# Kernel optimization log

Measured on AMD Instinct MI355X. Metric: run time of the kernel, lower is better.

## Reference

```python
import jax, jax.numpy as jnp
import numpy as np

N_NODES = 100000
N_EDGES = 1600000
N_GRAPHS = 256
F_IN = 38
HID = 64


def graph_conv(x, edge_index, w_rel, b_rel, w_root):
    # PyG GraphConv (aggr='add'): out = lin_rel(sum_{j in N(i)} x_j) + lin_root(x_i)
    src, dst = edge_index[0], edge_index[1]
    agg = jax.ops.segment_sum(x[src], dst, num_segments=N_NODES)  # [N, F]
    return agg @ w_rel + b_rel + x @ w_root


def setup_inputs() -> dict:
    key = jax.random.key(0)
    ks = jax.random.split(key, 10)
    x = jax.random.normal(ks[0], (N_NODES, F_IN), dtype=jnp.float32)
    edge_index = jax.random.randint(ks[1], (2, N_EDGES), 0, N_NODES, dtype=jnp.int64)
    batch = jnp.sort(jax.random.randint(ks[2], (N_NODES,), 0, N_GRAPHS, dtype=jnp.int64))
    s1 = 1.0 / np.sqrt(F_IN)
    s2 = 1.0 / np.sqrt(HID)
    w1_rel = jax.random.uniform(ks[3], (F_IN, HID), jnp.float32, -s1, s1)
    b1_rel = jax.random.uniform(ks[4], (HID,), jnp.float32, -s1, s1)
    w1_root = jax.random.uniform(ks[5], (F_IN, HID), jnp.float32, -s1, s1)
    w2_rel = jax.random.uniform(ks[6], (HID, HID), jnp.float32, -s2, s2)
    b2_rel = jax.random.uniform(ks[7], (HID,), jnp.float32, -s2, s2)
    w2_root = jax.random.uniform(ks[8], (HID, HID), jnp.float32, -s2, s2)
    return {"x": x, "edge_index": edge_index, "batch": batch,
            "w1_rel": w1_rel, "b1_rel": b1_rel, "w1_root": w1_root,
            "w2_rel": w2_rel, "b2_rel": b2_rel, "w2_root": w2_root}


def reference(x, edge_index, batch, w1_rel, b1_rel, w1_root, w2_rel, b2_rel, w2_root):
    h = graph_conv(x, edge_index, w1_rel, b1_rel, w1_root)
    h = jax.nn.relu(h)
    h = graph_conv(h, edge_index, w2_rel, b2_rel, w2_root)
    # global_mean_pool: segment mean over batch ids
    sums = jax.ops.segment_sum(h, batch, num_segments=N_GRAPHS)  # [G, HID]
    counts = jax.ops.segment_sum(jnp.ones((N_NODES,), h.dtype), batch, num_segments=N_GRAPHS)
    pooled = sums / jnp.maximum(counts, 1.0)[:, None]
    # dropout(p=0.5, training=False) is identity in eval mode
    return jax.nn.relu(pooled)
```

## Files before the change

### kernel.cpp

```cpp
#include <hip/hip_runtime.h>

#define N_NODES 100000
#define N_EDGES 1600000
#define N_GRAPHS 256
#define F_IN 38
#define F_PAD 40
#define HID 64
#define CAPD 48

#define NB   391
#define EPB  4096
#define EDGE_BLOCKS 391
#define PACK_BLOCKS 1024
#define PACK_CHUNKS ((N_NODES + 1) * F_PAD / 8)
#define BCAP 4608
#define NBL  (2 * NB)

typedef unsigned short ushort;
typedef unsigned int uint;
typedef _Float16 h2 __attribute__((ext_vector_type(2)));

__device__ __forceinline__ h2 u2h(uint u) {
    union { uint u; h2 h; } v; v.u = u; return v.h;
}
__device__ __forceinline__ uint h2u(h2 h) {
    union { uint u; h2 h; } v; v.h = h; return v.u;
}
__device__ __forceinline__ ushort f2h_bits(float f) {
    union { _Float16 h; ushort s; } v; v.h = (_Float16)f; return v.s;
}
__device__ __forceinline__ int clampi(int v) {
    return (int)min((uint)v, (uint)N_NODES);
}

__global__ __launch_bounds__(256, 4) void pre_kernel(
        const float* __restrict__ x,
        const int* __restrict__ src,
        const int* __restrict__ dst,
        int* __restrict__ gcur,
        uint* __restrict__ ebuf,
        ushort* __restrict__ xb,
        ushort* __restrict__ hb) {
    __shared__ int    hist[NB];
    __shared__ int    offs[NB];
    __shared__ int    cur[NB];
    __shared__ int    gbase[NB];
    __shared__ int    scan[512];
    __shared__ uint   sbuf[EPB];
    __shared__ ushort sb[EPB];

    const int blk = blockIdx.x;
    if (blk >= EDGE_BLOCKS) {
        int gid = (blk - EDGE_BLOCKS) * 256 + threadIdx.x;
        if (gid < HID) hb[(N_NODES << 6) + gid] = 0;
        const int stride = PACK_BLOCKS * 256;
        for (int c = gid; c < PACK_CHUNKS; c += stride) {
            int n = c / 5;
            int f0 = (c - n * 5) * 8;
            ushort u[8];
            #pragma unroll
            for (int j = 0; j < 8; ++j) {
                int f = f0 + j;
                float v = (n < N_NODES && f < F_IN) ? x[n * F_IN + f] : 0.0f;
                u[j] = f2h_bits(v);
            }
            uint4 pk;
            pk.x = (uint)u[0] | ((uint)u[1] << 16);
            pk.y = (uint)u[2] | ((uint)u[3] << 16);
            pk.z = (uint)u[4] | ((uint)u[5] << 16);
            pk.w = (uint)u[6] | ((uint)u[7] << 16);
            *(uint4*)(xb + c * 8) = pk;
        }
        return;
    }

    for (int i = threadIdx.x; i < NB; i += 256) hist[i] = 0;
    __syncthreads();

    const int base = blk * EPB + threadIdx.x;
    int  bkt[EPB / 256];
    uint pl[EPB / 256];
    #pragma unroll
    for (int i = 0; i < EPB / 256; ++i) {
        int e = base + i * 256;
        bkt[i] = -1;
        if (e < N_EDGES) {
            int d = dst[e];
            bkt[i] = d >> 8;
            pl[i] = ((uint)src[e] << 8) | ((uint)d & 255u);
            atomicAdd(&hist[bkt[i]], 1);
        }
    }
    __syncthreads();

    {
        int i0 = threadIdx.x, i1 = threadIdx.x + 256;
        scan[i0] = (i0 < NB) ? hist[i0] : 0;
        scan[i1] = (i1 < NB) ? hist[i1] : 0;
        __syncthreads();
        for (int d = 1; d < 512; d <<= 1) {
            int v0 = (i0 >= d) ? scan[i0 - d] : 0;
            int v1 = (i1 >= d) ? scan[i1 - d] : 0;
            __syncthreads();
            scan[i0] += v0;
            scan[i1] += v1;
            __syncthreads();
        }
    }
    for (int i = threadIdx.x; i < NB; i += 256) {
        int h = hist[i];
        int o = scan[i] - h;
        offs[i] = o;
        cur[i] = o;
        gbase[i] = (h > 0) ? atomicAdd(&gcur[i], h) : 0;
    }
    __syncthreads();

    #pragma unroll
    for (int i = 0; i < EPB / 256; ++i) {
        if (bkt[i] >= 0) {
            int pos = atomicAdd(&cur[bkt[i]], 1);
            sbuf[pos] = pl[i];
            sb[pos] = (ushort)bkt[i];
        }
    }
    __syncthreads();

    int total = scan[NB - 1];
    for (int i = threadIdx.x; i < total; i += 256) {
        int b = sb[i];
        int p = gbase[b] + (i - offs[b]);
        if (p < BCAP) ebuf[b * BCAP + p] = sbuf[i];
    }
}

__global__ __launch_bounds__(512, 8) void layer1_kernel(
        const uint* __restrict__ xb32,
        const uint* __restrict__ ebuf,
        const int* __restrict__ gcur,
        const float* __restrict__ w_rel,
        const float* __restrict__ b_rel,
        const float* __restrict__ w_root,
        const int* __restrict__ batch,
        ushort* __restrict__ hb,
        float* __restrict__ hsum) {
    __shared__ uint s_wrelp[20 * HID];
    __shared__ uint s_wrootp[20 * HID];
    __shared__ int  s_slots[128 * CAPD];
    __shared__ int  cl[128];

    for (int i = threadIdx.x; i < 20 * HID; i += 512) {
        int kk = i >> 6, cc = i & 63;
        int k0 = 2 * kk, k1 = 2 * kk + 1;
        float r0 = (k0 < F_IN) ? w_rel[k0 * HID + cc] : 0.f;
        float r1 = (k1 < F_IN) ? w_rel[k1 * HID + cc] : 0.f;
        float o0 = (k0 < F_IN) ? w_root[k0 * HID + cc] : 0.f;
        float o1 = (k1 < F_IN) ? w_root[k1 * HID + cc] : 0.f;
        s_wrelp[i]  = (uint)f2h_bits(r0) | ((uint)f2h_bits(r1) << 16);
        s_wrootp[i] = (uint)f2h_bits(o0) | ((uint)f2h_bits(o1) << 16);
    }
    const int b   = blockIdx.x >> 1;
    const int dlo = (blockIdx.x & 1) << 7;
    if (threadIdx.x < 128) cl[threadIdx.x] = 0;
    {
        int4* sp = (int4*)s_slots;
        int4 dummy = make_int4(N_NODES, N_NODES, N_NODES, N_NODES);
        for (int i = threadIdx.x; i < 128 * CAPD / 4; i += 512) sp[i] = dummy;
    }
    __syncthreads();
    int e1 = gcur[b]; if (e1 > BCAP) e1 = BCAP;
    for (int idx = threadIdx.x; idx < e1; idx += 512) {
        uint e = ebuf[b * BCAP + idx];
        int dl = (int)(e & 255u) - dlo;
        if ((uint)dl < 128u) {
            int pos = atomicAdd(&cl[dl], 1);
            if (pos < CAPD) s_slots[dl * CAPD + pos] = (int)(e >> 8);
        }
    }
    __syncthreads();

    const int wave = threadIdx.x >> 6, lane = threadIdx.x & 63;
    const int half = lane >> 5, l32 = lane & 31;
    const int nbase = (b << 8) + dlo;

    h2   sums[8];
    uint xvs[8];
    #pragma unroll
    for (int i = 0; i < 8; ++i) {
        int nl = wave * 16 + 2 * i + half;
        int n = nbase + nl;
        uint xv = 0;
        int dp = 0;
        if (n < N_NODES) {
            int deg = cl[nl]; if (deg > CAPD) deg = CAPD;
            dp = (deg + 15) & ~15; if (dp > CAPD) dp = CAPD;
            if (l32 < 20) xv = xb32[n * 20 + l32];
        }
        h2 sum = {(_Float16)0, (_Float16)0};
        const int* sl = s_slots + nl * CAPD;
        for (int j = 0; j < dp; j += 16) {
            int4 a4 = *(const int4*)(sl + j);
            int4 b4 = *(const int4*)(sl + j + 4);
            int4 c4 = *(const int4*)(sl + j + 8);
            int4 d4 = *(const int4*)(sl + j + 12);
            if (l32 < 20) {
                uint v0 = xb32[clampi(a4.x) * 20 + l32];
                uint v1 = xb32[clampi(a4.y) * 20 + l32];
                uint v2 = xb32[clampi(a4.z) * 20 + l32];
                uint v3 = xb32[clampi(a4.w) * 20 + l32];
                uint v4 = xb32[clampi(b4.x) * 20 + l32];
                uint v5 = xb32[clampi(b4.y) * 20 + l32];
                uint v6 = xb32[clampi(b4.z) * 20 + l32];
                uint v7 = xb32[clampi(b4.w) * 20 + l32];
                uint v8 = xb32[clampi(c4.x) * 20 + l32];
                uint v9 = xb32[clampi(c4.y) * 20 + l32];
                uint va = xb32[clampi(c4.z) * 20 + l32];
                uint vb = xb32[clampi(c4.w) * 20 + l32];
                uint vc = xb32[clampi(d4.x) * 20 + l32];
                uint vd = xb32[clampi(d4.y) * 20 + l32];
                uint ve = xb32[clampi(d4.z) * 20 + l32];
                uint vf = xb32[clampi(d4.w) * 20 + l32];
                h2 t0 = (u2h(v0) + u2h(v1)) + (u2h(v2) + u2h(v3));
                h2 t1 = (u2h(v4) + u2h(v5)) + (u2h(v6) + u2h(v7));
                h2 t2 = (u2h(v8) + u2h(v9)) + (u2h(va) + u2h(vb));
                h2 t3 = (u2h(vc) + u2h(vd)) + (u2h(ve) + u2h(vf));
                sum += (t0 + t1) + (t2 + t3);
            }
        }
        sums[i] = sum;
        xvs[i] = xv;
    }
    __syncthreads();
    uint* s_a = (uint*)s_slots;
    uint* s_x = ((uint*)s_slots) + 128 * 20;
    #pragma unroll
    for (int i = 0; i < 8; ++i) {
        int nl = wave * 16 + 2 * i + half;
        if (l32 < 20) {
            s_a[nl * 20 + l32] = h2u(sums[i]);
            s_x[nl * 20 + l32] = xvs[i];
        }
    }
    __syncthreads();

    const int c = lane, r = wave;
    const float bias = b_rel[c];
    float psum = 0.f;
    int cur_g = -1;
    for (int i = 0; i < 16; ++i) {
        int nl = r * 16 + i;
        int n = nbase + nl;
        if (n >= N_NODES) break;
        h2 acc = {(_Float16)0, (_Float16)0};
        #pragma unroll
        for (int k8 = 0; k8 < 5; ++k8) {
            uint4 pa = *(const uint4*)&s_a[nl * 20 + k8 * 4];
            uint4 px = *(const uint4*)&s_x[nl * 20 + k8 * 4];
            acc += u2h(pa.x) * u2h(s_wrelp[(k8 * 4 + 0) * HID + c]);
            acc += u2h(pa.y) * u2h(s_wrelp[(k8 * 4 + 1) * HID + c]);
            acc += u2h(pa.z) * u2h(s_wrelp[(k8 * 4 + 2) * HID + c]);
            acc += u2h(pa.w) * u2h(s_wrelp[(k8 * 4 + 3) * HID + c]);
            acc += u2h(px.x) * u2h(s_wrootp[(k8 * 4 + 0) * HID + c]);
            acc += u2h(px.y) * u2h(s_wrootp[(k8 * 4 + 1) * HID + c]);
            acc += u2h(px.z) * u2h(s_wrootp[(k8 * 4 + 2) * HID + c]);
            acc += u2h(px.w) * u2h(s_wrootp[(k8 * 4 + 3) * HID + c]);
        }
        float hv = fmaxf((float)acc.x + (float)acc.y + bias, 0.f);
        hb[(n << 6) + c] = f2h_bits(hv);
        int g = batch[n];
        if (g != cur_g) {
            if (cur_g >= 0) atomicAdd(&hsum[(cur_g << 6) + c], psum);
            psum = 0.f;
            cur_g = g;
        }
        psum += hv;
    }
    if (cur_g >= 0) atomicAdd(&hsum[(cur_g << 6) + c], psum);
}

__global__ __launch_bounds__(512, 8) void layer2_kernel(
        const uint* __restrict__ hb32,
        const uint* __restrict__ ebuf,
        const int* __restrict__ gcur,
        const int* __restrict__ batch,
        float* __restrict__ esum) {
    __shared__ int s_slots[128 * CAPD];
    __shared__ int cl[128];

    const int b   = blockIdx.x >> 1;
    const int dlo = (blockIdx.x & 1) << 7;
    if (threadIdx.x < 128) cl[threadIdx.x] = 0;
    {
        int4* sp = (int4*)s_slots;
        int4 dummy = make_int4(N_NODES, N_NODES, N_NODES, N_NODES);
        for (int i = threadIdx.x; i < 128 * CAPD / 4; i += 512) sp[i] = dummy;
    }
    __syncthreads();
    int e1 = gcur[b]; if (e1 > BCAP) e1 = BCAP;
    for (int idx = threadIdx.x; idx < e1; idx += 512) {
        uint e = ebuf[b * BCAP + idx];
        int dl = (int)(e & 255u) - dlo;
        if ((uint)dl < 128u) {
            int pos = atomicAdd(&cl[dl], 1);
            if (pos < CAPD) s_slots[dl * CAPD + pos] = (int)(e >> 8);
        }
    }
    __syncthreads();

    const int wave = threadIdx.x >> 6, lane = threadIdx.x & 63;
    const int half = lane >> 5, l32 = lane & 31;
    const int nbase = (b << 8) + dlo;

    float psum0 = 0.f, psum1 = 0.f;
    int cur_g = -1;
    for (int i = 0; i < 8; ++i) {
        int nl = wave * 16 + 2 * i + half;
        int n = nbase + nl;
        if (n < N_NODES) {
            int deg = cl[nl]; if (deg > CAPD) deg = CAPD;
            int dp = (deg + 15) & ~15; if (dp > CAPD) dp = CAPD;
            h2 sum = {(_Float16)0, (_Float16)0};
            const int* sl = s_slots + nl * CAPD;
            for (int j = 0; j < dp; j += 16) {
                int4 a4 = *(const int4*)(sl + j);
                int4 b4 = *(const int4*)(sl + j + 4);
                int4 c4 = *(const int4*)(sl + j + 8);
                int4 d4 = *(const int4*)(sl + j + 12);
                uint v0 = hb32[(clampi(a4.x) << 5) + l32];
                uint v1 = hb32[(clampi(a4.y) << 5) + l32];
                uint v2 = hb32[(clampi(a4.z) << 5) + l32];
                uint v3 = hb32[(clampi(a4.w) << 5) + l32];
                uint v4 = hb32[(clampi(b4.x) << 5) + l32];
                uint v5 = hb32[(clampi(b4.y) << 5) + l32];
                uint v6 = hb32[(clampi(b4.z) << 5) + l32];
                uint v7 = hb32[(clampi(b4.w) << 5) + l32];
                uint v8 = hb32[(clampi(c4.x) << 5) + l32];
                uint v9 = hb32[(clampi(c4.y) << 5) + l32];
                uint va = hb32[(clampi(c4.z) << 5) + l32];
                uint vb = hb32[(clampi(c4.w) << 5) + l32];
                uint vc = hb32[(clampi(d4.x) << 5) + l32];
                uint vd = hb32[(clampi(d4.y) << 5) + l32];
                uint ve = hb32[(clampi(d4.z) << 5) + l32];
                uint vf = hb32[(clampi(d4.w) << 5) + l32];
                h2 t0 = (u2h(v0) + u2h(v1)) + (u2h(v2) + u2h(v3));
                h2 t1 = (u2h(v4) + u2h(v5)) + (u2h(v6) + u2h(v7));
                h2 t2 = (u2h(v8) + u2h(v9)) + (u2h(va) + u2h(vb));
                h2 t3 = (u2h(vc) + u2h(vd)) + (u2h(ve) + u2h(vf));
                sum += (t0 + t1) + (t2 + t3);
            }
            int g = batch[n];
            if (g != cur_g) {
                if (cur_g >= 0) {
                    atomicAdd(&esum[(cur_g << 6) + 2 * l32], psum0);
                    atomicAdd(&esum[(cur_g << 6) + 2 * l32 + 1], psum1);
                }
                psum0 = 0.f; psum1 = 0.f;
                cur_g = g;
            }
            psum0 += (float)sum.x;
            psum1 += (float)sum.y;
        }
    }
    if (cur_g >= 0) {
        atomicAdd(&esum[(cur_g << 6) + 2 * l32], psum0);
        atomicAdd(&esum[(cur_g << 6) + 2 * l32 + 1], psum1);
    }
}

__global__ void finalize_kernel(const float* __restrict__ esum,
                                const float* __restrict__ hsum,
                                const float* __restrict__ w2_rel,
                                const float* __restrict__ w2_root,
                                const float* __restrict__ b2,
                                const int* __restrict__ batch,
                                float* __restrict__ out) {
    __shared__ float s_e[HID];
    __shared__ float s_h[HID];
    const int g = blockIdx.x;
    const int c = threadIdx.x;
    s_e[c] = esum[(g << 6) + c];
    s_h[c] = hsum[(g << 6) + c];
    __syncthreads();

    int lo = 0, hi = N_NODES;
    while (lo < hi) { int m = (lo + hi) >> 1; if (batch[m] < g) lo = m + 1; else hi = m; }
    int start = lo;
    hi = N_NODES;
    while (lo < hi) { int m = (lo + hi) >> 1; if (batch[m] < g + 1) lo = m + 1; else hi = m; }
    int cntg = lo - start;

    float acc = (float)cntg * b2[c];
    #pragma unroll
    for (int k = 0; k < HID; ++k) {
        acc += s_e[k] * w2_rel[k * HID + c];
        acc += s_h[k] * w2_root[k * HID + c];
    }
    float denom = cntg > 0 ? (float)cntg : 1.f;
    out[(g << 6) + c] = fmaxf(acc / denom, 0.f);
}

extern "C" void kernel_launch(void* const* d_in, const int* in_sizes, int n_in,
                              void* d_out, int out_size, void* d_ws, size_t ws_size,
                              hipStream_t stream) {
    const float* x       = (const float*)d_in[0];
    const int*   ei      = (const int*)  d_in[1];
    const int*   batch   = (const int*)  d_in[2];
    const float* w1_rel  = (const float*)d_in[3];
    const float* b1_rel  = (const float*)d_in[4];
    const float* w1_root = (const float*)d_in[5];
    const float* w2_rel  = (const float*)d_in[6];
    const float* b2_rel  = (const float*)d_in[7];
    const float* w2_root = (const float*)d_in[8];
    float* out = (float*)d_out;

    const int* src = ei;
    const int* dst = ei + N_EDGES;

    char* wsb = (char*)d_ws;
    float*  hsum  = (float*) (wsb);
    float*  esum  = (float*) (wsb + 65536);
    int*    gcur  = (int*)   (wsb + 131072);
    uint*   ebuf  = (uint*)  (wsb + 132672);
    ushort* xb    = (ushort*)(wsb + 19732640);
    ushort* hb    = (ushort*)(wsb + 27732720);

    hipMemsetAsync(wsb, 0, 132636, stream);

    {
        pre_kernel<<<EDGE_BLOCKS + PACK_BLOCKS, 256, 0, stream>>>(
            x, src, dst, gcur, ebuf, xb, hb);
    }
    {
        layer1_kernel<<<NBL, 512, 0, stream>>>((const uint*)xb, ebuf, gcur,
                                               w1_rel, b1_rel, w1_root, batch,
                                               hb, hsum);
    }
    {
        layer2_kernel<<<NBL, 512, 0, stream>>>((const uint*)hb, ebuf, gcur,
                                               batch, esum);
    }
    {
        finalize_kernel<<<N_GRAPHS, HID, 0, stream>>>(esum, hsum, w2_rel, w2_root,
                                                      b2_rel, batch, out);
    }
}
```

Before: 227.2 us.

## Replace per-block edge sort with two-pass histogram bucketing over 64 blocks

The edge-bucketing part of the preprocessing kernel changes from 391 blocks, each doing a local histogram, prefix scan and shared-memory sort over 4096 edges, to 64 blocks that each histogram a large edge range and then scatter directly to global buckets through shared atomic cursors. This removes the scan, the shared staging buffers and many syncs, and uses vectorized int4 loads. In exchange, dst is read twice, the global writes are scattered and less coalesced, and fewer blocks handle the edges, so parallelism in that phase drops. Edge order within buckets is now nondeterministic.

```diff
diff --git a/kernel.cpp b/kernel.cpp
--- a/kernel.cpp
+++ b/kernel.cpp
@@ -9,8 +9,8 @@
 #define CAPD 48
 
 #define NB   391
-#define EPB  4096
-#define EDGE_BLOCKS 391
+#define SBLK 64
+#define SEPB (N_EDGES / SBLK)
 #define PACK_BLOCKS 1024
 #define PACK_CHUNKS ((N_NODES + 1) * F_PAD / 8)
 #define BCAP 4608
@@ -33,7 +33,7 @@
     return (int)min((uint)v, (uint)N_NODES);
 }
 
-__global__ __launch_bounds__(256, 4) void pre_kernel(
+__global__ __launch_bounds__(256, 8) void pre_kernel(
         const float* __restrict__ x,
         const int* __restrict__ src,
         const int* __restrict__ dst,
@@ -41,17 +41,12 @@
         uint* __restrict__ ebuf,
         ushort* __restrict__ xb,
         ushort* __restrict__ hb) {
-    __shared__ int    hist[NB];
-    __shared__ int    offs[NB];
-    __shared__ int    cur[NB];
-    __shared__ int    gbase[NB];
-    __shared__ int    scan[512];
-    __shared__ uint   sbuf[EPB];
-    __shared__ ushort sb[EPB];
+    __shared__ int hist[NB];
+    __shared__ int cur[NB];
 
     const int blk = blockIdx.x;
-    if (blk >= EDGE_BLOCKS) {
-        int gid = (blk - EDGE_BLOCKS) * 256 + threadIdx.x;
+    if (blk >= SBLK) {
+        int gid = (blk - SBLK) * 256 + threadIdx.x;
         if (gid < HID) hb[(N_NODES << 6) + gid] = 0;
         const int stride = PACK_BLOCKS * 256;
         for (int c = gid; c < PACK_CHUNKS; c += stride) {
@@ -77,60 +72,41 @@
     for (int i = threadIdx.x; i < NB; i += 256) hist[i] = 0;
     __syncthreads();
 
-    const int base = blk * EPB + threadIdx.x;
-    int  bkt[EPB / 256];
-    uint pl[EPB / 256];
-    #pragma unroll
-    for (int i = 0; i < EPB / 256; ++i) {
-        int e = base + i * 256;
-        bkt[i] = -1;
-        if (e < N_EDGES) {
-            int d = dst[e];
-            bkt[i] = d >> 8;
-            pl[i] = ((uint)src[e] << 8) | ((uint)d & 255u);
-            atomicAdd(&hist[bkt[i]], 1);
-        }
-    }
-    __syncthreads();
-
-    {
-        int i0 = threadIdx.x, i1 = threadIdx.x + 256;
-        scan[i0] = (i0 < NB) ? hist[i0] : 0;
-        scan[i1] = (i1 < NB) ? hist[i1] : 0;
-        __syncthreads();
-        for (int d = 1; d < 512; d <<= 1) {
-            int v0 = (i0 >= d) ? scan[i0 - d] : 0;
-            int v1 = (i1 >= d) ? scan[i1 - d] : 0;
-            __syncthreads();
-            scan[i0] += v0;
-            scan[i1] += v1;
-            __syncthreads();
-        }
-    }
+    const int v0 = blk * (SEPB / 4);
+    const int v1 = v0 + SEPB / 4;
+    const int4* d4p = (const int4*)dst;
+    const int4* s4p = (const int4*)src;
+
+    for (int v = v0 + threadIdx.x; v < v1; v += 256) {
+        int4 d4 = d4p[v];
+        atomicAdd(&hist[d4.x >> 8], 1);
+        atomicAdd(&hist[d4.y >> 8], 1);
+        atomicAdd(&hist[d4.z >> 8], 1);
+        atomicAdd(&hist[d4.w >> 8], 1);
+    }
+    __syncthreads();
+
     for (int i = threadIdx.x; i < NB; i += 256) {
         int h = hist[i];
-        int o = scan[i] - h;
-        offs[i] = o;
-        cur[i] = o;
-        gbase[i] = (h > 0) ? atomicAdd(&gcur[i], h) : 0;
-    }
-    __syncthreads();
-
-    #pragma unroll
-    for (int i = 0; i < EPB / 256; ++i) {
-        if (bkt[i] >= 0) {
-            int pos = atomicAdd(&cur[bkt[i]], 1);
-            sbuf[pos] = pl[i];
-            sb[pos] = (ushort)bkt[i];
-        }
-    }
-    __syncthreads();
-
-    int total = scan[NB - 1];
-    for (int i = threadIdx.x; i < total; i += 256) {
-        int b = sb[i];
-        int p = gbase[b] + (i - offs[b]);
-        if (p < BCAP) ebuf[b * BCAP + p] = sbuf[i];
+        cur[i] = (h > 0) ? atomicAdd(&gcur[i], h) : 0;
+    }
+    __syncthreads();
+
+    for (int v = v0 + threadIdx.x; v < v1; v += 256) {
+        int4 d4 = d4p[v];
+        int4 s4 = s4p[v];
+        int b0 = d4.x >> 8;
+        int p0 = atomicAdd(&cur[b0], 1);
+        if (p0 < BCAP) ebuf[b0 * BCAP + p0] = ((uint)s4.x << 8) | ((uint)d4.x & 255u);
+        int b1 = d4.y >> 8;
+        int p1 = atomicAdd(&cur[b1], 1);
+        if (p1 < BCAP) ebuf[b1 * BCAP + p1] = ((uint)s4.y << 8) | ((uint)d4.y & 255u);
+        int b2 = d4.z >> 8;
+        int p2 = atomicAdd(&cur[b2], 1);
+        if (p2 < BCAP) ebuf[b2 * BCAP + p2] = ((uint)s4.z << 8) | ((uint)d4.z & 255u);
+        int b3 = d4.w >> 8;
+        int p3 = atomicAdd(&cur[b3], 1);
+        if (p3 < BCAP) ebuf[b3 * BCAP + p3] = ((uint)s4.w << 8) | ((uint)d4.w & 255u);
     }
 }
 
@@ -427,7 +403,7 @@
     hipMemsetAsync(wsb, 0, 132636, stream);
 
     {
-        pre_kernel<<<EDGE_BLOCKS + PACK_BLOCKS, 256, 0, stream>>>(
+        pre_kernel<<<SBLK + PACK_BLOCKS, 256, 0, stream>>>(
             x, src, dst, gcur, ebuf, xb, hb);
     }
     {
```

New measurement: 239.8 us. 5.5% more time.

## Reduce layer-2 aggregation directly per graph using src-partitioned edge buckets

Applied to the files above, without the earlier changes.

Layer-2 output is only needed after mean pooling, so the neighbour sum is reduced straight into per-graph totals. Edges are first bucketed by graph of the destination and by source-node partition, so each block sums h rows for one (graph, partition) pair. This removes per-node slot building and the per-node pooling in layer 2, and keeps the gathered rows within a smaller L2-resident range. The cost is an extra bucketing pass in pre_kernel and a new scatter kernel. It also adds fixed capacity limits per bucket and reuses the hb buffer region for temporary edge storage.

```diff
diff --git a/kernel.cpp b/kernel.cpp
--- a/kernel.cpp
+++ b/kernel.cpp
@@ -16,6 +16,12 @@
 #define BCAP 4608
 #define NBL  (2 * NB)
 
+#define NPART 8
+#define PDIV  12500
+#define PCAP  204800
+#define GCHUNKS 50
+#define GCAP3 1024
+
 typedef unsigned short ushort;
 typedef unsigned int uint;
 typedef _Float16 h2 __attribute__((ext_vector_type(2)));
@@ -37,8 +43,11 @@
         const float* __restrict__ x,
         const int* __restrict__ src,
         const int* __restrict__ dst,
+        const int* __restrict__ batch,
         int* __restrict__ gcur,
+        int* __restrict__ gcurp,
         uint* __restrict__ ebuf,
+        uint* __restrict__ ebufp,
         ushort* __restrict__ xb,
         ushort* __restrict__ hb) {
     __shared__ int    hist[NB];
@@ -50,7 +59,7 @@
     __shared__ ushort sb[EPB];
 
     const int blk = blockIdx.x;
-    if (blk >= EDGE_BLOCKS) {
+    if (blk >= EDGE_BLOCKS && blk < EDGE_BLOCKS + PACK_BLOCKS) {
         int gid = (blk - EDGE_BLOCKS) * 256 + threadIdx.x;
         if (gid < HID) hb[(N_NODES << 6) + gid] = 0;
         const int stride = PACK_BLOCKS * 256;
@@ -74,6 +83,53 @@
         return;
     }
 
+    if (blk >= EDGE_BLOCKS + PACK_BLOCKS) {
+        const int blk2 = blk - EDGE_BLOCKS - PACK_BLOCKS;
+        for (int i = threadIdx.x; i < NPART; i += 256) hist[i] = 0;
+        __syncthreads();
+        const int base = blk2 * EPB + threadIdx.x;
+        int  pp[EPB / 256];
+        uint pl[EPB / 256];
+        #pragma unroll
+        for (int i = 0; i < EPB / 256; ++i) {
+            int e = base + i * 256;
+            pp[i] = -1;
+            if (e < N_EDGES) {
+                int s = src[e];
+                int g = batch[dst[e]];
+                pp[i] = s / PDIV;
+                pl[i] = ((uint)s << 8) | (uint)g;
+                atomicAdd(&hist[pp[i]], 1);
+            }
+        }
+        __syncthreads();
+        if (threadIdx.x < NPART) {
+            int o = 0;
+            for (int j = 0; j < (int)threadIdx.x; ++j) o += hist[j];
+            offs[threadIdx.x] = o;
+            cur[threadIdx.x] = o;
+            int h = hist[threadIdx.x];
+            gbase[threadIdx.x] = (h > 0) ? atomicAdd(&gcurp[threadIdx.x], h) : 0;
+        }
+        __syncthreads();
+        #pragma unroll
+        for (int i = 0; i < EPB / 256; ++i) {
+            if (pp[i] >= 0) {
+                int pos = atomicAdd(&cur[pp[i]], 1);
+                sbuf[pos] = pl[i];
+                sb[pos] = (ushort)pp[i];
+            }
+        }
+        __syncthreads();
+        int total = offs[NPART - 1] + hist[NPART - 1];
+        for (int i = threadIdx.x; i < total; i += 256) {
+            int b = sb[i];
+            int p = gbase[b] + (i - offs[b]);
+            if (p < PCAP) ebufp[b * PCAP + p] = sbuf[i];
+        }
+        return;
+    }
+
     for (int i = threadIdx.x; i < NB; i += 256) hist[i] = 0;
     __syncthreads();
 
@@ -131,6 +187,79 @@
         int b = sb[i];
         int p = gbase[b] + (i - offs[b]);
         if (p < BCAP) ebuf[b * BCAP + p] = sbuf[i];
+    }
+}
+
+__global__ __launch_bounds__(256, 4) void scatter_g_kernel(
+        const uint* __restrict__ ebufp,
+        const int* __restrict__ gcurp,
+        int* __restrict__ gcur3,
+        uint* __restrict__ ebuf3) {
+    __shared__ int    hist[256];
+    __shared__ int    offs[256];
+    __shared__ int    cur[256];
+    __shared__ int    gbase[256];
+    __shared__ int    scan[256];
+    __shared__ uint   sbuf[EPB];
+    __shared__ ushort sb[EPB];
+
+    const int p = blockIdx.x & 7;
+    const int chunk = blockIdx.x >> 3;
+    int cnt_p = gcurp[p]; if (cnt_p > PCAP) cnt_p = PCAP;
+    const int e0 = chunk * EPB;
+    const int e1 = min(e0 + EPB, cnt_p);
+
+    hist[threadIdx.x] = 0;
+    __syncthreads();
+
+    int  gg[EPB / 256];
+    uint pl[EPB / 256];
+    #pragma unroll
+    for (int i = 0; i < EPB / 256; ++i) {
+        int idx = e0 + i * 256 + threadIdx.x;
+        gg[i] = -1;
+        if (idx < e1) {
+            uint v = ebufp[p * PCAP + idx];
+            gg[i] = (int)(v & 255u);
+            pl[i] = v;
+            atomicAdd(&hist[gg[i]], 1);
+        }
+    }
+    __syncthreads();
+
+    scan[threadIdx.x] = hist[threadIdx.x];
+    __syncthreads();
+    for (int d = 1; d < 256; d <<= 1) {
+        int v = (threadIdx.x >= (uint)d) ? scan[threadIdx.x - d] : 0;
+        __syncthreads();
+        scan[threadIdx.x] += v;
+        __syncthreads();
+    }
+    {
+        int h = hist[threadIdx.x];
+        int o = scan[threadIdx.x] - h;
+        offs[threadIdx.x] = o;
+        cur[threadIdx.x] = o;
+        gbase[threadIdx.x] = (h > 0)
+            ? atomicAdd(&gcur3[(threadIdx.x << 3) | p], h) : 0;
+    }
+    __syncthreads();
+
+    #pragma unroll
+    for (int i = 0; i < EPB / 256; ++i) {
+        if (gg[i] >= 0) {
+            int pos = atomicAdd(&cur[gg[i]], 1);
+            sbuf[pos] = pl[i];
+            sb[pos] = (ushort)gg[i];
+        }
+    }
+    __syncthreads();
+
+    int total = scan[255];
+    for (int i = threadIdx.x; i < total; i += 256) {
+        int g = sb[i];
+        int pos = gbase[g] + (i - offs[g]);
+        if (pos < GCAP3) ebuf3[((((uint)g << 3) | p) << 10) + pos] = sbuf[i];
     }
 }
 
@@ -278,92 +407,31 @@
     if (cur_g >= 0) atomicAdd(&hsum[(cur_g << 6) + c], psum);
 }
 
-__global__ __launch_bounds__(512, 8) void layer2_kernel(
+__global__ __launch_bounds__(256, 8) void layer2_kernel(
         const uint* __restrict__ hb32,
-        const uint* __restrict__ ebuf,
-        const int* __restrict__ gcur,
-        const int* __restrict__ batch,
+        const uint* __restrict__ ebuf3,
+        const int* __restrict__ gcur3,
         float* __restrict__ esum) {
-    __shared__ int s_slots[128 * CAPD];
-    __shared__ int cl[128];
-
-    const int b   = blockIdx.x >> 1;
-    const int dlo = (blockIdx.x & 1) << 7;
-    if (threadIdx.x < 128) cl[threadIdx.x] = 0;
-    {
-        int4* sp = (int4*)s_slots;
-        int4 dummy = make_int4(N_NODES, N_NODES, N_NODES, N_NODES);
-        for (int i = threadIdx.x; i < 128 * CAPD / 4; i += 512) sp[i] = dummy;
-    }
-    __syncthreads();
-    int e1 = gcur[b]; if (e1 > BCAP) e1 = BCAP;
-    for (int idx = threadIdx.x; idx < e1; idx += 512) {
-        uint e = ebuf[b * BCAP + idx];
-        int dl = (int)(e & 255u) - dlo;
-        if ((uint)dl < 128u) {
-            int pos = atomicAdd(&cl[dl], 1);
-            if (pos < CAPD) s_slots[dl * CAPD + pos] = (int)(e >> 8);
-        }
-    }
-    __syncthreads();
-
-    const int wave = threadIdx.x >> 6, lane = threadIdx.x & 63;
-    const int half = lane >> 5, l32 = lane & 31;
-    const int nbase = (b << 8) + dlo;
-
-    float psum0 = 0.f, psum1 = 0.f;
-    int cur_g = -1;
-    for (int i = 0; i < 8; ++i) {
-        int nl = wave * 16 + 2 * i + half;
-        int n = nbase + nl;
-        if (n < N_NODES) {
-            int deg = cl[nl]; if (deg > CAPD) deg = CAPD;
-            int dp = (deg + 15) & ~15; if (dp > CAPD) dp = CAPD;
-            h2 sum = {(_Float16)0, (_Float16)0};
-            const int* sl = s_slots + nl * CAPD;
-            for (int j = 0; j < dp; j += 16) {
-                int4 a4 = *(const int4*)(sl + j);
-                int4 b4 = *(const int4*)(sl + j + 4);
-                int4 c4 = *(const int4*)(sl + j + 8);
-                int4 d4 = *(const int4*)(sl + j + 12);
-                uint v0 = hb32[(clampi(a4.x) << 5) + l32];
-                uint v1 = hb32[(clampi(a4.y) << 5) + l32];
-                uint v2 = hb32[(clampi(a4.z) << 5) + l32];
-                uint v3 = hb32[(clampi(a4.w) << 5) + l32];
-                uint v4 = hb32[(clampi(b4.x) << 5) + l32];
-                uint v5 = hb32[(clampi(b4.y) << 5) + l32];
-                uint v6 = hb32[(clampi(b4.z) << 5) + l32];
-                uint v7 = hb32[(clampi(b4.w) << 5) + l32];
-                uint v8 = hb32[(clampi(c4.x) << 5) + l32];
-                uint v9 = hb32[(clampi(c4.y) << 5) + l32];
-                uint va = hb32[(clampi(c4.z) << 5) + l32];
-                uint vb = hb32[(clampi(c4.w) << 5) + l32];
-                uint vc = hb32[(clampi(d4.x) << 5) + l32];
-                uint vd = hb32[(clampi(d4.y) << 5) + l32];
-                uint ve = hb32[(clampi(d4.z) << 5) + l32];
-                uint vf = hb32[(clampi(d4.w) << 5) + l32];
-                h2 t0 = (u2h(v0) + u2h(v1)) + (u2h(v2) + u2h(v3));
-                h2 t1 = (u2h(v4) + u2h(v5)) + (u2h(v6) + u2h(v7));
-                h2 t2 = (u2h(v8) + u2h(v9)) + (u2h(va) + u2h(vb));
-                h2 t3 = (u2h(vc) + u2h(vd)) + (u2h(ve) + u2h(vf));
-                sum += (t0 + t1) + (t2 + t3);
-            }
-            int g = batch[n];
-            if (g != cur_g) {
-                if (cur_g >= 0) {
-                    atomicAdd(&esum[(cur_g << 6) + 2 * l32], psum0);
-                    atomicAdd(&esum[(cur_g << 6) + 2 * l32 + 1], psum1);
-                }
-                psum0 = 0.f; psum1 = 0.f;
-                cur_g = g;
-            }
-            psum0 += (float)sum.x;
-            psum1 += (float)sum.y;
-        }
-    }
-    if (cur_g >= 0) {
-        atomicAdd(&esum[(cur_g << 6) + 2 * l32], psum0);
-        atomicAdd(&esum[(cur_g << 6) + 2 * l32 + 1], psum1);
+    const int b3 = blockIdx.x;
+    const int g = b3 >> 3;
+    int cnt = gcur3[b3]; if (cnt > GCAP3) cnt = GCAP3;
+    const uint* eb = ebuf3 + ((uint)b3 << 10);
+
+    const int slot = threadIdx.x >> 5;
+    const int l32 = threadIdx.x & 31;
+
+    float ps0 = 0.f, ps1 = 0.f;
+    #pragma unroll 4
+    for (int e = slot; e < cnt; e += 8) {
+        uint pl = eb[e];
+        int srcn = (int)(pl >> 8);
+        h2 hv = u2h(hb32[(srcn << 5) + l32]);
+        ps0 += (float)hv.x;
+        ps1 += (float)hv.y;
+    }
+    if (cnt > 0) {
+        atomicAdd(&esum[(g << 6) + 2 * l32], ps0);
+        atomicAdd(&esum[(g << 6) + 2 * l32 + 1], ps1);
     }
 }
 
@@ -420,15 +488,23 @@
     float*  hsum  = (float*) (wsb);
     float*  esum  = (float*) (wsb + 65536);
     int*    gcur  = (int*)   (wsb + 131072);
-    uint*   ebuf  = (uint*)  (wsb + 132672);
+    int*    gcurp = (int*)   (wsb + 132640);
+    int*    gcur3 = (int*)   (wsb + 132672);
+    uint*   ebuf  = (uint*)  (wsb + 140864);
+    uint*   ebuf3 = (uint*)  (wsb + 7348352);
     ushort* xb    = (ushort*)(wsb + 19732640);
     ushort* hb    = (ushort*)(wsb + 27732720);
-
-    hipMemsetAsync(wsb, 0, 132636, stream);
-
-    {
-        pre_kernel<<<EDGE_BLOCKS + PACK_BLOCKS, 256, 0, stream>>>(
-            x, src, dst, gcur, ebuf, xb, hb);
+    uint*   ebufp = (uint*)  (wsb + 27732720);
+
+    hipMemsetAsync(wsb, 0, 140864, stream);
+
+    {
+        pre_kernel<<<EDGE_BLOCKS + PACK_BLOCKS + EDGE_BLOCKS, 256, 0, stream>>>(
+            x, src, dst, batch, gcur, gcurp, ebuf, ebufp, xb, hb);
+    }
+    {
+        scatter_g_kernel<<<NPART * GCHUNKS, 256, 0, stream>>>(
+            ebufp, gcurp, gcur3, ebuf3);
     }
     {
         layer1_kernel<<<NBL, 512, 0, stream>>>((const uint*)xb, ebuf, gcur,
@@ -436,8 +512,8 @@
                                                hb, hsum);
     }
     {
-        layer2_kernel<<<NBL, 512, 0, stream>>>((const uint*)hb, ebuf, gcur,
-                                               batch, esum);
+        layer2_kernel<<<N_GRAPHS * NPART, 256, 0, stream>>>(
+            (const uint*)hb, ebuf3, gcur3, esum);
     }
     {
         finalize_kernel<<<N_GRAPHS, HID, 0, stream>>>(esum, hsum, w2_rel, w2_root,
```

New measurement: 238.7 us. 1.05x slower.

## Stream layer-2 edges directly into per-graph sums, skipping per-node slot bucketing

Applied to the files above, without the earlier changes.

Layer 2 only needs per-graph sums of aggregated neighbor features, so the kernel now walks each bucket's edge list directly. It maps each destination to its graph id through a shared-memory batch table and accumulates into up to four register slots per graph, with global atomics as the fallback. This removes the shared-memory slot construction, the CAPD degree cap, and the padded dummy loads. Work is split into four edge-range blocks per bucket of 256 threads, adding shuffles and per-edge branches, and accumulation moves from fp16 to fp32.

```diff
diff --git a/kernel.cpp b/kernel.cpp
--- a/kernel.cpp
+++ b/kernel.cpp
@@ -278,92 +278,76 @@
     if (cur_g >= 0) atomicAdd(&hsum[(cur_g << 6) + c], psum);
 }
 
-__global__ __launch_bounds__(512, 8) void layer2_kernel(
+__global__ __launch_bounds__(256, 8) void layer2_kernel(
         const uint* __restrict__ hb32,
         const uint* __restrict__ ebuf,
         const int* __restrict__ gcur,
         const int* __restrict__ batch,
         float* __restrict__ esum) {
-    __shared__ int s_slots[128 * CAPD];
-    __shared__ int cl[128];
-
-    const int b   = blockIdx.x >> 1;
-    const int dlo = (blockIdx.x & 1) << 7;
-    if (threadIdx.x < 128) cl[threadIdx.x] = 0;
-    {
-        int4* sp = (int4*)s_slots;
-        int4 dummy = make_int4(N_NODES, N_NODES, N_NODES, N_NODES);
-        for (int i = threadIdx.x; i < 128 * CAPD / 4; i += 512) sp[i] = dummy;
-    }
-    __syncthreads();
+    __shared__ int   s_batch[256];
+    __shared__ float s_acc[4 * 64];
+
+    const int b = blockIdx.x >> 2;
+    const int q = blockIdx.x & 3;
+    const int nbase = b << 8;
+    {
+        int n = nbase + threadIdx.x;
+        s_batch[threadIdx.x] = (n < N_NODES) ? batch[n] : (N_GRAPHS - 1);
+    }
+    s_acc[threadIdx.x] = 0.f;
+    __syncthreads();
+    const int g0 = s_batch[0];
+
     int e1 = gcur[b]; if (e1 > BCAP) e1 = BCAP;
-    for (int idx = threadIdx.x; idx < e1; idx += 512) {
-        uint e = ebuf[b * BCAP + idx];
-        int dl = (int)(e & 255u) - dlo;
-        if ((uint)dl < 128u) {
-            int pos = atomicAdd(&cl[dl], 1);
-            if (pos < CAPD) s_slots[dl * CAPD + pos] = (int)(e >> 8);
-        }
-    }
-    __syncthreads();
+    const int lo = (e1 * q) >> 2;
+    const int hi = (e1 * (q + 1)) >> 2;
 
     const int wave = threadIdx.x >> 6, lane = threadIdx.x & 63;
-    const int half = lane >> 5, l32 = lane & 31;
-    const int nbase = (b << 8) + dlo;
-
-    float psum0 = 0.f, psum1 = 0.f;
-    int cur_g = -1;
-    for (int i = 0; i < 8; ++i) {
-        int nl = wave * 16 + 2 * i + half;
-        int n = nbase + nl;
-        if (n < N_NODES) {
-            int deg = cl[nl]; if (deg > CAPD) deg = CAPD;
-            int dp = (deg + 15) & ~15; if (dp > CAPD) dp = CAPD;
-            h2 sum = {(_Float16)0, (_Float16)0};
-            const int* sl = s_slots + nl * CAPD;
-            for (int j = 0; j < dp; j += 16) {
-                int4 a4 = *(const int4*)(sl + j);
-                int4 b4 = *(const int4*)(sl + j + 4);
-                int4 c4 = *(const int4*)(sl + j + 8);
-                int4 d4 = *(const int4*)(sl + j + 12);
-                uint v0 = hb32[(clampi(a4.x) << 5) + l32];
-                uint v1 = hb32[(clampi(a4.y) << 5) + l32];
-                uint v2 = hb32[(clampi(a4.z) << 5) + l32];
-                uint v3 = hb32[(clampi(a4.w) << 5) + l32];
-                uint v4 = hb32[(clampi(b4.x) << 5) + l32];
-                uint v5 = hb32[(clampi(b4.y) << 5) + l32];
-                uint v6 = hb32[(clampi(b4.z) << 5) + l32];
-                uint v7 = hb32[(clampi(b4.w) << 5) + l32];
-                uint v8 = hb32[(clampi(c4.x) << 5) + l32];
-                uint v9 = hb32[(clampi(c4.y) << 5) + l32];
-                uint va = hb32[(clampi(c4.z) << 5) + l32];
-                uint vb = hb32[(clampi(c4.w) << 5) + l32];
-                uint vc = hb32[(clampi(d4.x) << 5) + l32];
-                uint vd = hb32[(clampi(d4.y) << 5) + l32];
-                uint ve = hb32[(clampi(d4.z) << 5) + l32];
-                uint vf = hb32[(clampi(d4.w) << 5) + l32];
-                h2 t0 = (u2h(v0) + u2h(v1)) + (u2h(v2) + u2h(v3));
-                h2 t1 = (u2h(v4) + u2h(v5)) + (u2h(v6) + u2h(v7));
-                h2 t2 = (u2h(v8) + u2h(v9)) + (u2h(va) + u2h(vb));
-                h2 t3 = (u2h(vc) + u2h(vd)) + (u2h(ve) + u2h(vf));
-                sum += (t0 + t1) + (t2 + t3);
+    const int hf = lane >> 5, l32 = lane & 31;
+    const uint* eb = ebuf + b * BCAP;
+
+    float a0x = 0.f, a0y = 0.f, a1x = 0.f, a1y = 0.f;
+    float a2x = 0.f, a2y = 0.f, a3x = 0.f, a3y = 0.f;
+
+    for (int base = lo + (wave << 6); base < hi; base += 256) {
+        int cnt = hi - base; if (cnt > 64) cnt = 64;
+        uint pv = (lane < cnt) ? eb[base + lane] : 0u;
+        #pragma unroll 8
+        for (int k = 0; k < 32; ++k) {
+            int idx2 = 2 * k + hf;
+            uint p = __shfl(pv, idx2, 64);
+            if (idx2 < cnt) {
+                int srcn = (int)(p >> 8);
+                int g = s_batch[p & 255u];
+                int off = g - g0;
+                h2 hv = u2h(hb32[(srcn << 5) + l32]);
+                float hx = (float)hv.x, hy = (float)hv.y;
+                if (off == 0)      { a0x += hx; a0y += hy; }
+                else if (off == 1) { a1x += hx; a1y += hy; }
+                else if (off == 2) { a2x += hx; a2y += hy; }
+                else if (off == 3) { a3x += hx; a3y += hy; }
+                else {
+                    atomicAdd(&esum[(g << 6) + 2 * l32], hx);
+                    atomicAdd(&esum[(g << 6) + 2 * l32 + 1], hy);
+                }
             }
-            int g = batch[n];
-            if (g != cur_g) {
-                if (cur_g >= 0) {
-                    atomicAdd(&esum[(cur_g << 6) + 2 * l32], psum0);
-                    atomicAdd(&esum[(cur_g << 6) + 2 * l32 + 1], psum1);
-                }
-                psum0 = 0.f; psum1 = 0.f;
-                cur_g = g;
-            }
-            psum0 += (float)sum.x;
-            psum1 += (float)sum.y;
-        }
-    }
-    if (cur_g >= 0) {
-        atomicAdd(&esum[(cur_g << 6) + 2 * l32], psum0);
-        atomicAdd(&esum[(cur_g << 6) + 2 * l32 + 1], psum1);
+        }
+    }
+    atomicAdd(&s_acc[0 * 64 + 2 * l32],     a0x);
+    atomicAdd(&s_acc[0 * 64 + 2 * l32 + 1], a0y);
+    atomicAdd(&s_acc[1 * 64 + 2 * l32],     a1x);
+    atomicAdd(&s_acc[1 * 64 + 2 * l32 + 1], a1y);
+    atomicAdd(&s_acc[2 * 64 + 2 * l32],     a2x);
+    atomicAdd(&s_acc[2 * 64 + 2 * l32 + 1], a2y);
+    atomicAdd(&s_acc[3 * 64 + 2 * l32],     a3x);
+    atomicAdd(&s_acc[3 * 64 + 2 * l32 + 1], a3y);
+    __syncthreads();
+    {
+        int off = threadIdx.x >> 6, ch = threadIdx.x & 63;
+        int g = g0 + off;
+        float v = s_acc[off * 64 + ch];
+        if (v != 0.f && g < N_GRAPHS)
+            atomicAdd(&esum[(g << 6) + ch], v);
     }
 }
 
@@ -436,8 +420,8 @@
                                                hb, hsum);
     }
     {
-        layer2_kernel<<<NBL, 512, 0, stream>>>((const uint*)hb, ebuf, gcur,
-                                               batch, esum);
+        layer2_kernel<<<4 * NB, 256, 0, stream>>>((const uint*)hb, ebuf, gcur,
+                                                  batch, esum);
     }
     {
         finalize_kernel<<<N_GRAPHS, HID, 0, stream>>>(esum, hsum, w2_rel, w2_root,
```

After: 253.7 us. +11.6%, slower.
